# Kernel tuning notes

Hardware: AMD Instinct MI355X
Metric: run time of the kernel (lower is better)

Reference implementation:

```python
import jax, jax.numpy as jnp
import numpy as np

HEADS = 10
L1, L2 = 3.0, 3.0
OBS_X, OBS_Y = 0.0, 7.0
R = 4.0


def _forward(x, mean, std, mean_label, std_label,
             W1, b1, W2, b2, W31, b31, W32, b32,
             W41, b41, W42, b42, W51, b51, W52, b52, wt):
    relu = jax.nn.relu
    B = x.shape[0]
    x0 = x * std + mean  # unnormalized state (theta1, w1, theta2, w2)
    # multi-branch MLP
    h1 = relu(x @ W1.T + b1)
    h2 = relu(h1 @ W2.T + b2)
    h31 = relu(h2 @ W31.T + b31)
    h32 = relu(h2 @ W32.T + b32)
    h41 = relu(h31 @ W41.T + b41)
    h42 = relu(h32 @ W42.T + b42)
    x51 = h41 @ W51.T + b51                      # (B, 2*HEADS) per-head refs
    x52 = 4.0 * jax.nn.sigmoid(h42 @ W52.T + b52)  # (B, HEADS+1) CBF class-K gains

    th1, w1v, th2, w2v = x0[:, 0], x0[:, 1], x0[:, 2], x0[:, 3]
    s1, c1 = jnp.sin(th1), jnp.cos(th1)
    s2, c2 = jnp.sin(th2), jnp.cos(th2)
    px = L1 * c1 + L2 * c2 - OBS_X
    py = L1 * s1 + L2 * s2 - OBS_Y
    vx = -L1 * s1 * w1v - L2 * s2 * w2v
    vy = L1 * c1 * w1v + L2 * c2 * w2v
    barrier = px * px + py * py - R * R
    b_dot = 2.0 * px * vx + 2.0 * py * vy
    Lf2b = (2.0 * vx * vx + 2.0 * vy * vy
            + 2.0 * px * (-L1 * c1 * w1v ** 2 - L2 * c2 * w2v ** 2)
            + 2.0 * py * (-L1 * s1 * w1v ** 2 - L2 * s2 * w2v ** 2))
    g1 = 2.0 * px * (-L1 * s1) + 2.0 * py * (L1 * c1)
    g2 = 2.0 * px * (-L2 * s2) + 2.0 * py * (L2 * c2)
    G = -jnp.stack([g1, g2], axis=1)  # (B, 2), single inequality row per sample

    ref = jnp.transpose(x51.reshape(B, HEADS, 2), (1, 0, 2))  # (HEADS, B, 2)
    alpha = x52[:, 0:1]           # (B, 1)
    betas = x52[:, 1:]            # (B, HEADS)
    # h[k, b] = Lf2b + (a+bk)*b_dot + a*bk*barrier
    h = (Lf2b[:, None] + (alpha + betas) * b_dot[:, None]
         + alpha * betas * barrier[:, None]).T  # (HEADS, B)

    # QP: min 0.5||u||^2 + ref^T u  s.t.  G u <= h   (Q = I, 1 constraint)
    # closed form: u = -ref - max(0, (G.(-ref) - h)/(G.G)) * G
    u_unc = -ref                                  # (HEADS, B, 2)
    Gdot = jnp.sum(G * G, axis=1)                 # (B,)
    viol = jnp.einsum('hbc,bc->hb', u_unc, G) - h
    lam = jnp.maximum(viol / Gdot[None, :], 0.0)
    sol = u_unc - lam[..., None] * G[None, :, :]  # (HEADS, B, 2)

    wv = jax.nn.softmax(wt)                       # (HEADS,)
    rt = jnp.einsum('h,hbc->bc', wv, sol)         # (B, 2)
    return (rt - mean_label) / std_label


def setup_inputs() -> dict:
    key = jax.random.key(0)
    B = 16384
    dims = [4, 2048, 2048, 1024, 1024, 1024, 1024, 2]
    ks = jax.random.split(key, 10)

    def lin(k, fin, fout):
        kw, kb = jax.random.split(k)
        W = jax.random.normal(kw, (fout, fin), jnp.float32) / jnp.sqrt(float(fin))
        b = 0.01 * jax.random.normal(kb, (fout,), jnp.float32)
        return W, b

    W1, b1 = lin(ks[0], dims[0], dims[1])
    W2, b2 = lin(ks[1], dims[1], dims[2])
    W31, b31 = lin(ks[2], dims[2], dims[3])
    W32, b32 = lin(ks[3], dims[2], dims[4])
    W41, b41 = lin(ks[4], dims[3], dims[5])
    W42, b42 = lin(ks[5], dims[4], dims[6])
    W51, b51 = lin(ks[6], dims[5], dims[7] * HEADS)
    W52, b52 = lin(ks[7], dims[6], HEADS + 1)
    wt = jnp.ones((HEADS,), jnp.float32)
    x = jax.random.normal(ks[8], (B, dims[0]), jnp.float32)
    return {
        'x': x, 'sgn': 1,
        'mean': jnp.zeros((4,), jnp.float32), 'std': jnp.ones((4,), jnp.float32),
        'mean_label': jnp.zeros((2,), jnp.float32), 'std_label': jnp.ones((2,), jnp.float32),
        'W1': W1, 'b1': b1, 'W2': W2, 'b2': b2, 'W31': W31, 'b31': b31,
        'W32': W32, 'b32': b32, 'W41': W41, 'b41': b41, 'W42': W42, 'b42': b42,
        'W51': W51, 'b51': b51, 'W52': W52, 'b52': b52, 'wt': wt,
    }


def reference(x, sgn, mean, std, mean_label, std_label,
              W1, b1, W2, b2, W31, b31, W32, b32,
              W41, b41, W42, b42, W51, b51, W52, b52, wt):
    del sgn  # unused in the training (batched QP) path
    return _forward(x, mean, std, mean_label, std_label,
                    W1, b1, W2, b2, W31, b31, W32, b32,
                    W41, b41, W42, b42, W51, b51, W52, b52, wt)
```

## Files before the change

kernel.cpp:

```cpp
#include <hip/hip_runtime.h>

typedef unsigned short u16;
typedef unsigned char  u8;
typedef unsigned int   u32;
typedef __attribute__((ext_vector_type(8)))  short short8;
typedef __attribute__((ext_vector_type(16))) float floatx16;
typedef __attribute__((ext_vector_type(4)))  int   intx4;
typedef __attribute__((ext_vector_type(16))) int   intx16;
typedef __attribute__((ext_vector_type(8)))  u16   u16x8;
typedef __attribute__((ext_vector_type(4)))  u16   u16x4;

__device__ __forceinline__ u16 f2b(float f) {
    u32 u = __float_as_uint(f);
    u = (u + 0x7FFFu + ((u >> 16) & 1u)) >> 16;
    return (u16)u;
}
__device__ __forceinline__ float b2f(u16 h) {
    return __uint_as_float(((u32)h) << 16);
}
__device__ __forceinline__ int q8(float v, float inv) {
    return __float2int_rn(fminf(fmaxf(v * inv, -127.f), 127.f));
}

__device__ __forceinline__ void pad_block(const float* __restrict__ Wsrc, int rows,
                                          u16* __restrict__ Wdst,
                                          const float* __restrict__ bsrc,
                                          float* __restrict__ bdst, int blk) {
    int i = blk * 256 + threadIdx.x;
    int idx = i * 4;
    int r = idx >> 10;
    int c = idx & 1023;
    u16x4 o;
    if (r < rows) {
        float4 v = *(const float4*)&Wsrc[r * 1024 + c];
        o[0] = f2b(v.x); o[1] = f2b(v.y); o[2] = f2b(v.z); o[3] = f2b(v.w);
    } else {
        o[0] = 0; o[1] = 0; o[2] = 0; o[3] = 0;
    }
    *(u16x4*)&Wdst[idx] = o;
    if (i < 128) bdst[i] = (i < rows) ? bsrc[i] : 0.f;
}

__device__ __forceinline__ void wquant_row(const float* __restrict__ src,
                                           int K, u8* __restrict__ dstrow,
                                           float* __restrict__ sW,
                                           float* __restrict__ Wsum, int row_out) {
    const int lane = threadIdx.x & 63;
    const int iters = K >> 8;
    float mx = 0.f;
    for (int i = 0; i < iters; ++i) {
        float4 v = *(const float4*)&src[i * 256 + lane * 4];
        mx = fmaxf(mx, fmaxf(fmaxf(fabsf(v.x), fabsf(v.y)),
                             fmaxf(fabsf(v.z), fabsf(v.w))));
    }
#pragma unroll
    for (int off = 32; off >= 1; off >>= 1) mx = fmaxf(mx, __shfl_xor(mx, off));
    float sw  = fmaxf(mx * (1.f / 127.f), 1e-20f);
    float inv = 1.f / sw;
    int ssum = 0;
    for (int i = 0; i < iters; ++i) {
        float4 v = *(const float4*)&src[i * 256 + lane * 4];
        int q0 = q8(v.x, inv), q1 = q8(v.y, inv), q2 = q8(v.z, inv), q3 = q8(v.w, inv);
        ssum += q0 + q1 + q2 + q3;
        u32 p = (q0 & 255) | ((q1 & 255) << 8) | ((q2 & 255) << 16) | ((q3 & 255) << 24);
        *(u32*)&dstrow[i * 256 + lane * 4] = p;
    }
#pragma unroll
    for (int off = 32; off >= 1; off >>= 1) ssum += __shfl_xor(ssum, off);
    if (lane == 0) { sW[row_out] = sw; Wsum[row_out] = sw * (float)ssum; }
}

__device__ __forceinline__ void l1q_block(const float* __restrict__ x,
                                          const float* __restrict__ W1,
                                          const float* __restrict__ b1,
                                          u8* __restrict__ h1q,
                                          float* __restrict__ sA,
                                          float* __restrict__ muA, int blk) {
    __shared__ float wmx[4], wmn[4];
    const int t    = threadIdx.x;
    const int wave = t >> 6;
    const int lane = t & 63;
    const int b0 = blk * 16;
    const int n0 = t * 8;
    float4 wreg[8]; float breg[8];
    const float4* W14 = (const float4*)W1;
#pragma unroll
    for (int i = 0; i < 8; ++i) { wreg[i] = W14[n0 + i]; breg[i] = b1[n0 + i]; }
    for (int r = 0; r < 16; ++r) {
        int b = b0 + r;
        float4 xv = ((const float4*)x)[b];
        float v[8];
        float lmx = 0.f, lmn = 3.4e38f;
#pragma unroll
        for (int i = 0; i < 8; ++i) {
            float s = xv.x * wreg[i].x + xv.y * wreg[i].y +
                      xv.z * wreg[i].z + xv.w * wreg[i].w + breg[i];
            s = fmaxf(s, 0.f);
            v[i] = s;
            lmx = fmaxf(lmx, s); lmn = fminf(lmn, s);
        }
#pragma unroll
        for (int off = 32; off >= 1; off >>= 1) {
            lmx = fmaxf(lmx, __shfl_xor(lmx, off));
            lmn = fminf(lmn, __shfl_xor(lmn, off));
        }
        if (lane == 0) { wmx[wave] = lmx; wmn[wave] = lmn; }
        __syncthreads();
        float mx = fmaxf(fmaxf(wmx[0], wmx[1]), fmaxf(wmx[2], wmx[3]));
        float mn = fminf(fminf(wmn[0], wmn[1]), fminf(wmn[2], wmn[3]));
        float mu  = 0.5f * (mx + mn);
        float s   = fmaxf((mx - mn) * (1.f / 254.f), 1e-20f);
        float inv = 1.f / s;
        int q[8];
#pragma unroll
        for (int i = 0; i < 8; ++i) q[i] = q8(v[i] - mu, inv);
        uint2 p;
        p.x = (q[0] & 255) | ((q[1] & 255) << 8) | ((q[2] & 255) << 16) | ((q[3] & 255) << 24);
        p.y = (q[4] & 255) | ((q[5] & 255) << 8) | ((q[6] & 255) << 16) | ((q[7] & 255) << 24);
        *(uint2*)&h1q[(size_t)b * 2048 + n0] = p;
        if (t == 0) { sA[b] = s; muA[b] = mu; }
        __syncthreads();
    }
}

__global__ __launch_bounds__(256)
void k_prep1(const float* W2, u8* W2q, float* sW2, float* Wsum2,
             const float* x, const float* W1, const float* b1,
             u8* h1q, float* sA1, float* muA1,
             const float* W31, const float* W32, u8* W3q, float* sW3, float* Wsum3,
             const float* W41, u8* W41q, float* sW41, float* Ws41,
             const float* W42, u8* W42q, float* sW42, float* Ws42,
             const float* W51, u16* W51p, const float* b51, float* b51p,
             const float* W52, u16* W52p, const float* b52, float* b52p,
             const float* b31, const float* b32, float* b3c) {
    int blk = blockIdx.x;
    if (blk < 512) {
        int row = blk * 4 + (threadIdx.x >> 6);
        wquant_row(W2 + (size_t)row * 2048, 2048, W2q + (size_t)row * 2048,
                   sW2, Wsum2, row);
        return;
    }
    blk -= 512;
    if (blk < 1024) { l1q_block(x, W1, b1, h1q, sA1, muA1, blk); return; }
    blk -= 1024;
    if (blk < 512) {
        int row = blk * 4 + (threadIdx.x >> 6);
        const float* src = (row < 1024) ? W31 + (size_t)row * 2048
                                        : W32 + (size_t)(row - 1024) * 2048;
        wquant_row(src, 2048, W3q + (size_t)row * 2048, sW3, Wsum3, row);
        return;
    }
    blk -= 512;
    if (blk < 256) {
        int row = blk * 4 + (threadIdx.x >> 6);
        wquant_row(W41 + (size_t)row * 1024, 1024, W41q + (size_t)row * 1024,
                   sW41, Ws41, row);
        return;
    }
    blk -= 256;
    if (blk < 256) {
        int row = blk * 4 + (threadIdx.x >> 6);
        wquant_row(W42 + (size_t)row * 1024, 1024, W42q + (size_t)row * 1024,
                   sW42, Ws42, row);
        return;
    }
    blk -= 256;
    if (blk < 128) { pad_block(W51, 20, W51p, b51, b51p, blk); return; }
    blk -= 128;
    if (blk < 128) { pad_block(W52, 11, W52p, b52, b52p, blk); return; }
    blk -= 128;
    if (blk < 8) {
        int i = blk * 256 + threadIdx.x;
        b3c[i] = (i < 1024) ? b31[i] : b32[i - 1024];
    }
}

template<int NCH>
__global__ __launch_bounds__(256)
void k_aquant(const u16* __restrict__ src, u8* __restrict__ dst,
              float* __restrict__ s, float* __restrict__ mu) {
    const int wave = threadIdx.x >> 6;
    const int lane = threadIdx.x & 63;
    const int row  = blockIdx.x * 4 + wave;
    const int rowlen = NCH * 512;
    const u16* sr = src + (size_t)row * rowlen;
    u8*       dr  = dst + (size_t)row * rowlen;
    u16x8 vbuf[NCH];
    float mx = -3.4e38f, mn = 3.4e38f;
#pragma unroll
    for (int c = 0; c < NCH; ++c) {
        u16x8 v = *(const u16x8*)&sr[c * 512 + lane * 8];
        vbuf[c] = v;
#pragma unroll
        for (int i = 0; i < 8; ++i) {
            float f = b2f(v[i]);
            mx = fmaxf(mx, f); mn = fminf(mn, f);
        }
    }
#pragma unroll
    for (int off = 32; off >= 1; off >>= 1) {
        mx = fmaxf(mx, __shfl_xor(mx, off));
        mn = fminf(mn, __shfl_xor(mn, off));
    }
    float m  = 0.5f * (mx + mn);
    float sc = fmaxf((mx - mn) * (1.f / 254.f), 1e-20f);
    float inv = 1.f / sc;
#pragma unroll
    for (int c = 0; c < NCH; ++c) {
        u16x8 v = vbuf[c];
        int q[8];
#pragma unroll
        for (int i = 0; i < 8; ++i) q[i] = q8(b2f(v[i]) - m, inv);
        uint2 p;
        p.x = (q[0] & 255) | ((q[1] & 255) << 8) | ((q[2] & 255) << 16) | ((q[3] & 255) << 24);
        p.y = (q[4] & 255) | ((q[5] & 255) << 8) | ((q[6] & 255) << 16) | ((q[7] & 255) << 24);
        *(uint2*)&dr[c * 512 + lane * 8] = p;
    }
    if (lane == 0) { s[row] = sc; mu[row] = m; }
}

__global__ __launch_bounds__(256, 2)
void k_gemmq(const u8* __restrict__ A, const u8* __restrict__ Wq,
             const float* __restrict__ sA, const float* __restrict__ muA,
             const float* __restrict__ sW, const float* __restrict__ Wsum,
             const float* __restrict__ bias, u16* __restrict__ C,
             int K, int lda, int ldc, int sstride,
             const u8* A2, const u8* Wq2,
             const float* sA2, const float* muA2,
             const float* sW2, const float* Wsum2,
             const float* bias2, u16* C2, int split) {
    __shared__ __align__(16) u8 As[256 * 128];
    __shared__ __align__(16) u8 Ws[128 * 128];

    const int tid  = threadIdx.x;
    const int wave = tid >> 6;
    const int lane = tid & 63;

    int flat = blockIdx.y * gridDim.x + blockIdx.x;
    int xcd = flat & 7;
    int p   = flat >> 3;
    int bx  = p % gridDim.x;
    int by  = (p / gridDim.x) * 8 + xcd;
    if (A2 != nullptr && by >= split) {
        A = A2; Wq = Wq2; sA = sA2; muA = muA2; sW = sW2; Wsum = Wsum2;
        bias = bias2; C = C2; by -= split;
    }
    const int bm = by * 256;
    const int bn = bx * 128;

    const int srow = lane >> 3;
    const int sg   = ((lane & 7) ^ srow) * 16;

    const int wm    = (wave & 1) * 128;
    const int wn    = (wave >> 1) * 64;
    const int row32 = lane & 31;
    const int half  = lane >> 5;

    intx16 acc[4][2];
#pragma unroll
    for (int i = 0; i < 4; ++i)
#pragma unroll
        for (int j = 0; j < 2; ++j)
#pragma unroll
            for (int r = 0; r < 16; ++r) acc[i][j][r] = 0;

    for (int k0 = 0; k0 < K; k0 += 128) {
#pragma unroll
        for (int i = 0; i < 8; ++i) {
            int ci = wave * 8 + i;
            int r  = ci * 8 + srow;
            const u8* ga = A + (size_t)(bm + r) * lda + k0 + sg;
            __builtin_amdgcn_global_load_lds(
                (const __attribute__((address_space(1))) void*)ga,
                (__attribute__((address_space(3))) void*)&As[ci * 1024], 16, 0, 0);
        }
#pragma unroll
        for (int i = 0; i < 4; ++i) {
            int ci = wave * 4 + i;
            int r  = ci * 8 + srow;
            const u8* gw = Wq + (size_t)(bn + r) * K + k0 + sg;
            __builtin_amdgcn_global_load_lds(
                (const __attribute__((address_space(1))) void*)gw,
                (__attribute__((address_space(3))) void*)&Ws[ci * 1024], 16, 0, 0);
        }
        __syncthreads();

#pragma unroll
        for (int s = 0; s < 4; ++s) {
            const int c = s * 2 + half;
            intx4 af[4], bf[2];
#pragma unroll
            for (int i = 0; i < 4; ++i) {
                int r = wm + i * 32 + row32;
                af[i] = *(const intx4*)&As[r * 128 + ((c ^ (r & 7)) * 16)];
            }
#pragma unroll
            for (int j = 0; j < 2; ++j) {
                int r = wn + j * 32 + row32;
                bf[j] = *(const intx4*)&Ws[r * 128 + ((c ^ (r & 7)) * 16)];
            }
#pragma unroll
            for (int i = 0; i < 4; ++i)
#pragma unroll
                for (int j = 0; j < 2; ++j)
                    acc[i][j] = __builtin_amdgcn_mfma_i32_32x32x32_i8(
                        af[i], bf[j], acc[i][j], 0, 0, 0);
        }
        __syncthreads();
    }

    float sWv[2], Wsv[2], bv[2];
#pragma unroll
    for (int j = 0; j < 2; ++j) {
        int col = bn + wn + j * 32 + row32;
        sWv[j] = sW[col]; Wsv[j] = Wsum[col]; bv[j] = bias[col];
    }
#pragma unroll
    for (int i = 0; i < 4; ++i)
#pragma unroll
        for (int r = 0; r < 16; ++r) {
            int row = bm + wm + i * 32 + (r & 3) + 8 * (r >> 2) + 4 * half;
            float sa = sA[row * sstride], mu = muA[row * sstride];
#pragma unroll
            for (int j = 0; j < 2; ++j) {
                int col = bn + wn + j * 32 + row32;
                float v = (float)acc[i][j][r] * (sa * sWv[j]) + mu * Wsv[j] + bv[j];
                v = fmaxf(v, 0.f);
                C[(size_t)row * ldc + col] = f2b(v);
            }
        }
}

__global__ __launch_bounds__(256, 2)
void k_heads_final(const u16* __restrict__ hbuf,
                   const u16* __restrict__ W51p, const float* __restrict__ b51p,
                   const u16* __restrict__ W52p, const float* __restrict__ b52p,
                   const float* __restrict__ x, const float* __restrict__ mean,
                   const float* __restrict__ std_,
                   const float* __restrict__ mean_label,
                   const float* __restrict__ std_label,
                   const float* __restrict__ wt, float* __restrict__ out) {
    __shared__ __align__(16) u16 A1[128 * 64];
    __shared__ __align__(16) u16 A2[128 * 64];
    __shared__ __align__(16) u16 Wl[2][32 * 64];
    __shared__ float x51s[128 * 20];
    __shared__ float x52s[128 * 11];

    const int tid  = threadIdx.x;
    const int wave = tid >> 6;
    const int lane = tid & 63;
    const int bm   = blockIdx.x * 128;

    const int srow = lane >> 3;
    const int sg   = ((lane & 7) ^ srow) * 8;

    const int g     = wave >> 1;
    const int wm    = (wave & 1) * 64;
    const int row32 = lane & 31;
    const int half  = lane >> 5;

    const u16* Abase = hbuf + (g ? 1024 : 0);
    const u16* Wp    = g ? W52p : W51p;
    u16* Asl = g ? A2 : A1;

    floatx16 acc[2];
#pragma unroll
    for (int i = 0; i < 2; ++i)
#pragma unroll
        for (int r = 0; r < 16; ++r) acc[i][r] = 0.f;

    for (int k0 = 0; k0 < 1024; k0 += 64) {
#pragma unroll
        for (int i = 0; i < 8; ++i) {
            int rl = wm + i * 8 + srow;
            const u16* ga = Abase + (size_t)(bm + rl) * 2048 + k0 + sg;
            __builtin_amdgcn_global_load_lds(
                (const __attribute__((address_space(1))) void*)ga,
                (__attribute__((address_space(3))) void*)&Asl[(wm + i * 8) * 64],
                16, 0, 0);
        }
        if ((wave & 1) == 0) {
#pragma unroll
            for (int i = 0; i < 4; ++i) {
                int r = i * 8 + srow;
                const u16* gw = Wp + (size_t)r * 1024 + k0 + sg;
                __builtin_amdgcn_global_load_lds(
                    (const __attribute__((address_space(1))) void*)gw,
                    (__attribute__((address_space(3))) void*)&Wl[g][(i * 8) * 64],
                    16, 0, 0);
            }
        }
        __syncthreads();
#pragma unroll
        for (int s = 0; s < 4; ++s) {
            const int c = s * 2 + half;
            short8 a0, a1, bf;
            { int r = wm + row32;       a0 = *(const short8*)&Asl[r * 64 + ((c ^ (r & 7)) * 8)]; }
            { int r = wm + 32 + row32;  a1 = *(const short8*)&Asl[r * 64 + ((c ^ (r & 7)) * 8)]; }
            { int r = row32;            bf = *(const short8*)&Wl[g][r * 64 + ((c ^ (r & 7)) * 8)]; }
            acc[0] = __builtin_amdgcn_mfma_f32_32x32x16_bf16(a0, bf, acc[0], 0, 0, 0);
            acc[1] = __builtin_amdgcn_mfma_f32_32x32x16_bf16(a1, bf, acc[1], 0, 0, 0);
        }
        __syncthreads();
    }

    {
        int col = row32;
        int ncols = g ? 11 : 20;
        if (col < ncols) {
            float bj = (g ? b52p : b51p)[col];
            float* dst = g ? x52s : x51s;
#pragma unroll
            for (int i = 0; i < 2; ++i)
#pragma unroll
                for (int r = 0; r < 16; ++r) {
                    int row = wm + i * 32 + (r & 3) + 8 * (r >> 2) + 4 * half;
                    dst[row * ncols + col] = acc[i][r] + bj;
                }
        }
    }
    __syncthreads();

    if (tid < 128) {
        int b = bm + tid;

        float w[10], m = -1e30f;
#pragma unroll
        for (int h = 0; h < 10; ++h) { w[h] = wt[h]; m = fmaxf(m, w[h]); }
        float ssum = 0.f;
#pragma unroll
        for (int h = 0; h < 10; ++h) { w[h] = __expf(w[h] - m); ssum += w[h]; }
        float winv = 1.f / ssum;

        float4 xv = ((const float4*)x)[b];
        float th1 = xv.x * std_[0] + mean[0];
        float w1v = xv.y * std_[1] + mean[1];
        float th2 = xv.z * std_[2] + mean[2];
        float w2v = xv.w * std_[3] + mean[3];
        float s1 = sinf(th1), c1 = cosf(th1);
        float s2 = sinf(th2), c2 = cosf(th2);
        float px = 3.f * c1 + 3.f * c2 - 0.f;
        float py = 3.f * s1 + 3.f * s2 - 7.f;
        float vx = -3.f * s1 * w1v - 3.f * s2 * w2v;
        float vy =  3.f * c1 * w1v + 3.f * c2 * w2v;
        float barrier = px * px + py * py - 16.f;
        float b_dot = 2.f * (px * vx + py * vy);
        float Lf2b = 2.f * vx * vx + 2.f * vy * vy
                   + 2.f * px * (-3.f * c1 * w1v * w1v - 3.f * c2 * w2v * w2v)
                   + 2.f * py * (-3.f * s1 * w1v * w1v - 3.f * s2 * w2v * w2v);
        float g1 = 2.f * px * (-3.f * s1) + 2.f * py * (3.f * c1);
        float g2 = 2.f * px * (-3.f * s2) + 2.f * py * (3.f * c2);
        float Gx = -g1, Gy = -g2;
        float Gdot = Gx * Gx + Gy * Gy;

        float alpha = 4.f / (1.f + expf(-x52s[tid * 11 + 0]));

        float rx = 0.f, ry = 0.f;
#pragma unroll
        for (int h = 0; h < 10; ++h) {
            float r0 = x51s[tid * 20 + 2 * h];
            float r1 = x51s[tid * 20 + 2 * h + 1];
            float beta = 4.f / (1.f + expf(-x52s[tid * 11 + 1 + h]));
            float hh = Lf2b + (alpha + beta) * b_dot + alpha * beta * barrier;
            float ux = -r0, uy = -r1;
            float viol = ux * Gx + uy * Gy - hh;
            float lam = fmaxf(viol / Gdot, 0.f);
            float sx = ux - lam * Gx;
            float sy = uy - lam * Gy;
            float wk = w[h] * winv;
            rx += wk * sx; ry += wk * sy;
        }
        out[2 * b]     = (rx - mean_label[0]) / std_label[0];
        out[2 * b + 1] = (ry - mean_label[1]) / std_label[1];
    }
}

extern "C" void kernel_launch(void* const* d_in, const int* in_sizes, int n_in,
                              void* d_out, int out_size, void* d_ws, size_t ws_size,
                              hipStream_t stream) {
    const float* x    = (const float*)d_in[0];
    const float* mean = (const float*)d_in[2];
    const float* std_ = (const float*)d_in[3];
    const float* mean_label = (const float*)d_in[4];
    const float* std_label  = (const float*)d_in[5];
    const float* W1  = (const float*)d_in[6];
    const float* b1  = (const float*)d_in[7];
    const float* W2  = (const float*)d_in[8];
    const float* b2  = (const float*)d_in[9];
    const float* W31 = (const float*)d_in[10];
    const float* b31 = (const float*)d_in[11];
    const float* W32 = (const float*)d_in[12];
    const float* b32 = (const float*)d_in[13];
    const float* W41 = (const float*)d_in[14];
    const float* b41 = (const float*)d_in[15];
    const float* W42 = (const float*)d_in[16];
    const float* b42 = (const float*)d_in[17];
    const float* W51 = (const float*)d_in[18];
    const float* b51 = (const float*)d_in[19];
    const float* W52 = (const float*)d_in[20];
    const float* b52 = (const float*)d_in[21];
    const float* wt  = (const float*)d_in[22];

    const int B = in_sizes[0] / 4;

    char* wsp = (char*)d_ws;
    size_t off = 0;
    auto alloc = [&](size_t bytes) {
        void* p = wsp + off;
        off += (bytes + 255) & ~(size_t)255;
        return p;
    };
    u8*    W2q   = (u8*)   alloc((size_t)2048 * 2048);
    float* sW2   = (float*)alloc(2048 * 4);
    float* Wsum2 = (float*)alloc(2048 * 4);
    u8*    h1q   = (u8*)   alloc((size_t)B * 2048);
    float* sA1   = (float*)alloc((size_t)B * 4);
    float* muA1  = (float*)alloc((size_t)B * 4);
    u8*    W3q   = (u8*)   alloc((size_t)2048 * 2048);
    float* sW3   = (float*)alloc(2048 * 4);
    float* Wsum3 = (float*)alloc(2048 * 4);
    u8*    W41q  = (u8*)   alloc((size_t)1024 * 1024);
    float* sW41  = (float*)alloc(1024 * 4);
    float* Ws41  = (float*)alloc(1024 * 4);
    u8*    W42q  = (u8*)   alloc((size_t)1024 * 1024);
    float* sW42  = (float*)alloc(1024 * 4);
    float* Ws42  = (float*)alloc(1024 * 4);
    u16*   W51p  = (u16*)  alloc((size_t)128 * 1024 * 2);
    u16*   W52p  = (u16*)  alloc((size_t)128 * 1024 * 2);
    float* b51p  = (float*)alloc(512);
    float* b52p  = (float*)alloc(512);
    float* b3c   = (float*)alloc(2048 * 4);
    u8*    h2q   = (u8*)   alloc((size_t)B * 2048);
    float* s2a   = (float*)alloc((size_t)B * 4);
    float* mu2a  = (float*)alloc((size_t)B * 4);
    u8*    h34q  = (u8*)   alloc((size_t)B * 2048);
    float* s34   = (float*)alloc((size_t)2 * B * 4);
    float* mu34  = (float*)alloc((size_t)2 * B * 4);
    u16*   bufA  = (u16*)  alloc((size_t)B * 2048 * 2);
    u16*   bufB  = (u16*)  alloc((size_t)B * 2048 * 2);
    const u8* NUL8 = nullptr;

    k_prep1<<<2824, 256, 0, stream>>>(
        W2, W2q, sW2, Wsum2, x, W1, b1, h1q, sA1, muA1,
        W31, W32, W3q, sW3, Wsum3,
        W41, W41q, sW41, Ws41, W42, W42q, sW42, Ws42,
        W51, W51p, b51, b51p, W52, W52p, b52, b52p, b31, b32, b3c);

    k_gemmq<<<dim3(16, 64), 256, 0, stream>>>(
        h1q, W2q, sA1, muA1, sW2, Wsum2, b2, bufB, 2048, 2048, 2048, 1,
        NUL8, NUL8, nullptr, nullptr, nullptr, nullptr, nullptr, nullptr, 0);

    k_aquant<4><<<B / 4, 256, 0, stream>>>(bufB, h2q, s2a, mu2a);

    k_gemmq<<<dim3(16, 64), 256, 0, stream>>>(
        h2q, W3q, s2a, mu2a, sW3, Wsum3, b3c, bufA, 2048, 2048, 2048, 1,
        NUL8, NUL8, nullptr, nullptr, nullptr, nullptr, nullptr, nullptr, 0);

    k_aquant<2><<<2 * B / 4, 256, 0, stream>>>(bufA, h34q, s34, mu34);

    k_gemmq<<<dim3(8, 128), 256, 0, stream>>>(
        h34q, W41q, s34, mu34, sW41, Ws41, b41, bufB,
        1024, 2048, 2048, 2,
        h34q + 1024, W42q, s34 + 1, mu34 + 1, sW42, Ws42, b42, bufB + 1024, 64);

    k_heads_final<<<B / 128, 256, 0, stream>>>(
        bufB, W51p, b51p, W52p, b52p, x, mean, std_,
        mean_label, std_label, wt, (float*)d_out);
}
```

Baseline: 402.9 us.

## Defer weight quantization into preceding GEMM launches as extra blocks

Quantization of the later layers' weights (W31/W32, W41/W42) and padding of the head weights (W51/W52) move out of the prep kernel. They now run as extra blocks appended to the grid of the GEMM launch that comes before each layer uses them, so this memory-bound work can overlap the GEMM tail. The row quantizer is also templated on K and keeps the row in registers instead of reading it twice. The cost is a longer GEMM kernel signature and extra branching, and the spare blocks may compete with GEMM blocks for CUs.

```diff
diff --git a/kernel.cpp b/kernel.cpp
--- a/kernel.cpp
+++ b/kernel.cpp
@@ -41,26 +41,31 @@
     if (i < 128) bdst[i] = (i < rows) ? bsrc[i] : 0.f;
 }
 
-__device__ __forceinline__ void wquant_row(const float* __restrict__ src,
-                                           int K, u8* __restrict__ dstrow,
-                                           float* __restrict__ sW,
-                                           float* __restrict__ Wsum, int row_out) {
+template<int K>
+__device__ __forceinline__ void wquant_row_reg(const float* __restrict__ src,
+                                               u8* __restrict__ dstrow,
+                                               float* __restrict__ sW,
+                                               float* __restrict__ Wsum,
+                                               int row_out) {
     const int lane = threadIdx.x & 63;
-    const int iters = K >> 8;
+    constexpr int NV = K / 256;
+    float4 buf[NV];
     float mx = 0.f;
-    for (int i = 0; i < iters; ++i) {
-        float4 v = *(const float4*)&src[i * 256 + lane * 4];
-        mx = fmaxf(mx, fmaxf(fmaxf(fabsf(v.x), fabsf(v.y)),
-                             fmaxf(fabsf(v.z), fabsf(v.w))));
+#pragma unroll
+    for (int i = 0; i < NV; ++i) {
+        buf[i] = *(const float4*)&src[i * 256 + lane * 4];
+        mx = fmaxf(mx, fmaxf(fmaxf(fabsf(buf[i].x), fabsf(buf[i].y)),
+                             fmaxf(fabsf(buf[i].z), fabsf(buf[i].w))));
     }
 #pragma unroll
     for (int off = 32; off >= 1; off >>= 1) mx = fmaxf(mx, __shfl_xor(mx, off));
     float sw  = fmaxf(mx * (1.f / 127.f), 1e-20f);
     float inv = 1.f / sw;
     int ssum = 0;
-    for (int i = 0; i < iters; ++i) {
-        float4 v = *(const float4*)&src[i * 256 + lane * 4];
-        int q0 = q8(v.x, inv), q1 = q8(v.y, inv), q2 = q8(v.z, inv), q3 = q8(v.w, inv);
+#pragma unroll
+    for (int i = 0; i < NV; ++i) {
+        int q0 = q8(buf[i].x, inv), q1 = q8(buf[i].y, inv);
+        int q2 = q8(buf[i].z, inv), q3 = q8(buf[i].w, inv);
         ssum += q0 + q1 + q2 + q3;
         u32 p = (q0 & 255) | ((q1 & 255) << 8) | ((q2 & 255) << 16) | ((q3 & 255) << 24);
         *(u32*)&dstrow[i * 256 + lane * 4] = p;
@@ -127,48 +132,17 @@
 void k_prep1(const float* W2, u8* W2q, float* sW2, float* Wsum2,
              const float* x, const float* W1, const float* b1,
              u8* h1q, float* sA1, float* muA1,
-             const float* W31, const float* W32, u8* W3q, float* sW3, float* Wsum3,
-             const float* W41, u8* W41q, float* sW41, float* Ws41,
-             const float* W42, u8* W42q, float* sW42, float* Ws42,
-             const float* W51, u16* W51p, const float* b51, float* b51p,
-             const float* W52, u16* W52p, const float* b52, float* b52p,
              const float* b31, const float* b32, float* b3c) {
     int blk = blockIdx.x;
     if (blk < 512) {
         int row = blk * 4 + (threadIdx.x >> 6);
-        wquant_row(W2 + (size_t)row * 2048, 2048, W2q + (size_t)row * 2048,
-                   sW2, Wsum2, row);
+        wquant_row_reg<2048>(W2 + (size_t)row * 2048, W2q + (size_t)row * 2048,
+                             sW2, Wsum2, row);
         return;
     }
     blk -= 512;
     if (blk < 1024) { l1q_block(x, W1, b1, h1q, sA1, muA1, blk); return; }
     blk -= 1024;
-    if (blk < 512) {
-        int row = blk * 4 + (threadIdx.x >> 6);
-        const float* src = (row < 1024) ? W31 + (size_t)row * 2048
-                                        : W32 + (size_t)(row - 1024) * 2048;
-        wquant_row(src, 2048, W3q + (size_t)row * 2048, sW3, Wsum3, row);
-        return;
-    }
-    blk -= 512;
-    if (blk < 256) {
-        int row = blk * 4 + (threadIdx.x >> 6);
-        wquant_row(W41 + (size_t)row * 1024, 1024, W41q + (size_t)row * 1024,
-                   sW41, Ws41, row);
-        return;
-    }
-    blk -= 256;
-    if (blk < 256) {
-        int row = blk * 4 + (threadIdx.x >> 6);
-        wquant_row(W42 + (size_t)row * 1024, 1024, W42q + (size_t)row * 1024,
-                   sW42, Ws42, row);
-        return;
-    }
-    blk -= 256;
-    if (blk < 128) { pad_block(W51, 20, W51p, b51, b51p, blk); return; }
-    blk -= 128;
-    if (blk < 128) { pad_block(W52, 11, W52p, b52, b52p, blk); return; }
-    blk -= 128;
     if (blk < 8) {
         int i = blk * 256 + threadIdx.x;
         b3c[i] = (i < 1024) ? b31[i] : b32[i - 1024];
@@ -224,11 +198,51 @@
              const float* __restrict__ sA, const float* __restrict__ muA,
              const float* __restrict__ sW, const float* __restrict__ Wsum,
              const float* __restrict__ bias, u16* __restrict__ C,
-             int K, int lda, int ldc, int sstride,
+             int K, int lda, int ldc, int sstride, int gemmY,
              const u8* A2, const u8* Wq2,
              const float* sA2, const float* muA2,
              const float* sW2, const float* Wsum2,
-             const float* bias2, u16* C2, int split) {
+             const float* bias2, u16* C2, int split,
+             int bfmode,
+             const float* bfA_src, u8* bfA_dst, float* bfA_s, float* bfA_sum,
+             int bfA_K, int bfA_blocks,
+             const float* bfB_src, u8* bfB_dst, float* bfB_s, float* bfB_sum,
+             int bfB_K,
+             const float* pW1, u16* pD1, const float* pb1, float* pbd1,
+             const float* pW2, u16* pD2, const float* pb2, float* pbd2) {
+    const int ngemm = gemmY * gridDim.x;
+    int flat = blockIdx.y * gridDim.x + blockIdx.x;
+    if (flat >= ngemm) {
+        int pblk = flat - ngemm;
+        if (bfmode == 1) {
+            if (pblk < bfA_blocks) {
+                int row = pblk * 4 + (threadIdx.x >> 6);
+                if (bfA_K == 2048)
+                    wquant_row_reg<2048>(bfA_src + (size_t)row * 2048,
+                                         bfA_dst + (size_t)row * 2048,
+                                         bfA_s, bfA_sum, row);
+                else
+                    wquant_row_reg<1024>(bfA_src + (size_t)row * 1024,
+                                         bfA_dst + (size_t)row * 1024,
+                                         bfA_s, bfA_sum, row);
+            } else {
+                int row = (pblk - bfA_blocks) * 4 + (threadIdx.x >> 6);
+                if (bfB_K == 2048)
+                    wquant_row_reg<2048>(bfB_src + (size_t)row * 2048,
+                                         bfB_dst + (size_t)row * 2048,
+                                         bfB_s, bfB_sum, row);
+                else
+                    wquant_row_reg<1024>(bfB_src + (size_t)row * 1024,
+                                         bfB_dst + (size_t)row * 1024,
+                                         bfB_s, bfB_sum, row);
+            }
+        } else if (bfmode == 2) {
+            if (pblk < 128)      pad_block(pW1, 20, pD1, pb1, pbd1, pblk);
+            else if (pblk < 256) pad_block(pW2, 11, pD2, pb2, pbd2, pblk - 128);
+        }
+        return;
+    }
+
     __shared__ __align__(16) u8 As[256 * 128];
     __shared__ __align__(16) u8 Ws[128 * 128];
 
@@ -236,7 +250,6 @@
     const int wave = tid >> 6;
     const int lane = tid & 63;
 
-    int flat = blockIdx.y * gridDim.x + blockIdx.x;
     int xcd = flat & 7;
     int p   = flat >> 3;
     int bx  = p % gridDim.x;
@@ -540,28 +553,38 @@
     u16*   bufB  = (u16*)  alloc((size_t)B * 2048 * 2);
     const u8* NUL8 = nullptr;
 
-    k_prep1<<<2824, 256, 0, stream>>>(
-        W2, W2q, sW2, Wsum2, x, W1, b1, h1q, sA1, muA1,
-        W31, W32, W3q, sW3, Wsum3,
-        W41, W41q, sW41, Ws41, W42, W42q, sW42, Ws42,
-        W51, W51p, b51, b51p, W52, W52p, b52, b52p, b31, b32, b3c);
-
-    k_gemmq<<<dim3(16, 64), 256, 0, stream>>>(
-        h1q, W2q, sA1, muA1, sW2, Wsum2, b2, bufB, 2048, 2048, 2048, 1,
-        NUL8, NUL8, nullptr, nullptr, nullptr, nullptr, nullptr, nullptr, 0);
+    k_prep1<<<1544, 256, 0, stream>>>(W2, W2q, sW2, Wsum2,
+                                      x, W1, b1, h1q, sA1, muA1,
+                                      b31, b32, b3c);
+
+    k_gemmq<<<dim3(16, 64 + 32), 256, 0, stream>>>(
+        h1q, W2q, sA1, muA1, sW2, Wsum2, b2, bufB, 2048, 2048, 2048, 1, 64,
+        NUL8, NUL8, nullptr, nullptr, nullptr, nullptr, nullptr, nullptr, 0,
+        1,
+        W31, W3q, sW3, Wsum3, 2048, 256,
+        W32, W3q + (size_t)1024 * 2048, sW3 + 1024, Wsum3 + 1024, 2048,
+        nullptr, nullptr, nullptr, nullptr, nullptr, nullptr, nullptr, nullptr);
 
     k_aquant<4><<<B / 4, 256, 0, stream>>>(bufB, h2q, s2a, mu2a);
 
-    k_gemmq<<<dim3(16, 64), 256, 0, stream>>>(
-        h2q, W3q, s2a, mu2a, sW3, Wsum3, b3c, bufA, 2048, 2048, 2048, 1,
-        NUL8, NUL8, nullptr, nullptr, nullptr, nullptr, nullptr, nullptr, 0);
+    k_gemmq<<<dim3(16, 64 + 32), 256, 0, stream>>>(
+        h2q, W3q, s2a, mu2a, sW3, Wsum3, b3c, bufA, 2048, 2048, 2048, 1, 64,
+        NUL8, NUL8, nullptr, nullptr, nullptr, nullptr, nullptr, nullptr, 0,
+        1,
+        W41, W41q, sW41, Ws41, 1024, 256,
+        W42, W42q, sW42, Ws42, 1024,
+        nullptr, nullptr, nullptr, nullptr, nullptr, nullptr, nullptr, nullptr);
 
     k_aquant<2><<<2 * B / 4, 256, 0, stream>>>(bufA, h34q, s34, mu34);
 
-    k_gemmq<<<dim3(8, 128), 256, 0, stream>>>(
+    k_gemmq<<<dim3(8, 128 + 32), 256, 0, stream>>>(
         h34q, W41q, s34, mu34, sW41, Ws41, b41, bufB,
-        1024, 2048, 2048, 2,
-        h34q + 1024, W42q, s34 + 1, mu34 + 1, sW42, Ws42, b42, bufB + 1024, 64);
+        1024, 2048, 2048, 2, 128,
+        h34q + 1024, W42q, s34 + 1, mu34 + 1, sW42, Ws42, b42, bufB + 1024, 64,
+        2,
+        nullptr, nullptr, nullptr, nullptr, 0, 0,
+        nullptr, nullptr, nullptr, nullptr, 0,
+        W51, W51p, b51, b51p, W52, W52p, b52, b52p);
 
     k_heads_final<<<B / 128, 256, 0, stream>>>(
         bufB, W51p, b51p, W52p, b52p, x, mean, std_,
```

Result: no change. 410.3 us (+1.8%).
